# Kernel optimization log

Measured on AMD Instinct MI355X. Metric: run time of the kernel, lower is better.

The kernel has to match this reference:

```python
import jax, jax.numpy as jnp
import numpy as np

B, T, C, HS = 8, 4096, 512, 64

def setup_inputs() -> dict:
    key = jax.random.key(0)
    k1, k2, k3, k4 = jax.random.split(key, 4)
    x = jax.random.normal(k1, (B, T, C), dtype=jnp.float32)
    # causal mask (lower-triangular), int32: 1 = keep, 0 = mask out
    mask = jnp.tril(jnp.ones((T, T), dtype=jnp.int32))
    Wk = jax.random.normal(k2, (C, HS), dtype=jnp.float32) * (1.0 / np.sqrt(C))
    Wq = jax.random.normal(k3, (C, HS), dtype=jnp.float32) * (1.0 / np.sqrt(C))
    Wv = jax.random.normal(k4, (C, HS), dtype=jnp.float32) * (1.0 / np.sqrt(C))
    return {"x": x, "mask": mask, "Wk": Wk, "Wq": Wq, "Wv": Wv}

def reference(x, mask, Wk, Wq, Wv):
    # single self-attention head; scale uses C (n_embd), matching the source
    k = jnp.einsum('btc,ch->bth', x, Wk)   # [B,T,HS]
    q = jnp.einsum('btc,ch->bth', x, Wq)
    v = jnp.einsum('btc,ch->bth', x, Wv)
    scale = x.shape[-1] ** -0.5
    wei = jnp.einsum('bth,bsh->bts', q, k) * scale          # [B,T,T]
    wei = jnp.where(mask == 0, jnp.float32(-1e9), wei)
    wei = jax.nn.softmax(wei, axis=-1)
    # dropout is identity in eval mode
    out = jnp.einsum('bts,bsh->bth', wei, v)                # [B,T,HS]
    return out
```

## Files before the change

### kernel.cpp

```cpp
#include <hip/hip_runtime.h>
#include <hip/hip_bf16.h>
#include <stdint.h>

typedef unsigned short u16;
typedef __bf16 bf16x8_t __attribute__((ext_vector_type(8)));
typedef __bf16 bf16x4_t __attribute__((ext_vector_type(4)));
typedef float f32x4_t __attribute__((ext_vector_type(4)));
typedef float f32x8_t __attribute__((ext_vector_type(8)));
typedef float f32x16_t __attribute__((ext_vector_type(16)));
typedef int i32x2_t __attribute__((ext_vector_type(2)));

#define TSEQ 4096
#define CDIM 512
#define HSD  64
#define NBATCH 8

static __device__ __forceinline__ f32x4_t mfma16(bf16x8_t a, bf16x8_t b, f32x4_t c) {
  return __builtin_amdgcn_mfma_f32_16x16x32_bf16(a, b, c, 0, 0, 0);
}
static __device__ __forceinline__ f32x16_t mfma32(bf16x8_t a, bf16x8_t b, f32x16_t c) {
  return __builtin_amdgcn_mfma_f32_32x32x16_bf16(a, b, c, 0, 0, 0);
}

static __device__ __forceinline__ u16 f2bf(float f) {
  union { __bf16 h; u16 s; } v; v.h = (__bf16)f;
  return v.s;
}
static __device__ __forceinline__ float bf2f(u16 h) {
  union { unsigned u; float f; } v; v.u = ((unsigned)h) << 16;
  return v.f;
}
static __device__ __forceinline__ bf16x8_t pack8(const float* p) {
  f32x8_t v = *(const f32x8_t*)p;
  return __builtin_convertvector(v, bf16x8_t);
}
static __device__ __forceinline__ bf16x4_t cvt4(f32x4_t v) {
  return __builtin_convertvector(v, bf16x4_t);
}

static __device__ __forceinline__ void gload16(const void* g, void* l) {
  __builtin_amdgcn_global_load_lds(
      (const __attribute__((address_space(1))) unsigned int*)g,
      (__attribute__((address_space(3))) unsigned int*)l, 16, 0, 0);
}

#define QSCALE (0.044194173824159216f * 1.4426950408889634f)
#define MFIX 32.0f

__global__ __launch_bounds__(256) void repack_w(const float* __restrict__ Wk,
                                                const float* __restrict__ Wq,
                                                const float* __restrict__ Wv,
                                                u16* __restrict__ pw) {
  int i = blockIdx.x * 256 + threadIdx.x;
  int j    = i & 7;
  int l15  = (i >> 3) & 15;
  int quad = (i >> 7) & 3;
  int f    = i >> 9;
  int kc   = f / 12;
  int n12  = f - kc * 12;
  int m    = n12 >> 2;
  int n    = n12 & 3;
  const float* W = (m == 0) ? Wk : ((m == 1) ? Wq : Wv);
  pw[i] = f2bf(W[(kc * 32 + quad * 8 + j) * HSD + n * 16 + l15]);
}

__global__ __launch_bounds__(256, 2) void proj_kernel(const float* __restrict__ x,
                                                      const u16* __restrict__ pw,
                                                      u16* __restrict__ kb,
                                                      u16* __restrict__ qb,
                                                      u16* __restrict__ vb,
                                                      u16* __restrict__ vbT,
                                                      int split) {
  const int tid = threadIdx.x;
  const int lane = tid & 63;
  const int wave = tid >> 6;
  const int l15 = lane & 15, quad = lane >> 4;
  const int rblk = (int)blockIdx.x;
  const int rowLocal = wave * 16 + l15;

  __shared__ __align__(16) char SMEM[61440];
  float (*XS)[2048] = (float (*)[2048])SMEM;
  u16   (*PS)[6144] = (u16 (*)[6144])(SMEM + 24576);
  u16* VtS = (u16*)SMEM;

  const float* xg = x + (size_t)rblk * 64 * CDIM;

  const int xrow = tid >> 3;
  const int xch  = tid & 7;

  f32x4_t acc[12];
#pragma unroll
  for (int n = 0; n < 12; ++n) acc[n] = f32x4_t{0.f, 0.f, 0.f, 0.f};

  auto STAGE = [&](int slot, int kc) {
#pragma unroll
    for (int p = 0; p < 2; ++p) {
      const float* src = xg + (size_t)(p * 32 + xrow) * CDIM + kc * 32 + xch * 4;
      gload16(src, (char*)&XS[slot][0] + p * 4096 + tid * 16);
    }
#pragma unroll
    for (int r = 0; r < 3; ++r) {
      int f = r * 256 + tid;
      gload16(pw + (size_t)kc * 6144 + (size_t)f * 8, (char*)&PS[slot][0] + f * 16);
    }
  };

  STAGE(0, 0);
  STAGE(1, 1);

  int slot = 0;
  for (int kc = 0; kc < 16; ++kc) {
    if (kc < 15) asm volatile("s_waitcnt vmcnt(5)" ::: "memory");
    else         asm volatile("s_waitcnt vmcnt(0)" ::: "memory");
    __builtin_amdgcn_s_barrier();

    if (kc + 2 < 16) {
      int s2 = slot + 2; if (s2 >= 3) s2 -= 3;
      STAGE(s2, kc + 2);
    }

    f32x8_t xv = *(const f32x8_t*)&XS[slot][rowLocal * 32 + quad * 8];
    bf16x8_t a = __builtin_convertvector(xv, bf16x8_t);
#pragma unroll
    for (int n12 = 0; n12 < 12; ++n12) {
      bf16x8_t b = *(const bf16x8_t*)&PS[slot][((n12 * 4 + quad) * 16 + l15) * 8];
      acc[n12] = mfma16(a, b, acc[n12]);
    }

    ++slot; if (slot >= 3) slot = 0;
  }

  const int row_base = rblk * 64 + wave * 16 + quad * 4;
#pragma unroll
  for (int n = 0; n < 4; ++n) {
#pragma unroll
    for (int r = 0; r < 4; ++r) {
      kb[(size_t)(row_base + r) * HSD + n * 16 + l15] = f2bf(acc[n][r]);
      qb[(size_t)(row_base + r) * HSD + n * 16 + l15] = f2bf(acc[4 + n][r] * QSCALE);
    }
  }

  if (!split) {
#pragma unroll
    for (int n = 0; n < 4; ++n)
#pragma unroll
      for (int r = 0; r < 4; ++r)
        vb[(size_t)(row_base + r) * HSD + n * 16 + l15] = f2bf(acc[8 + n][r]);
  } else {
    __syncthreads();
#pragma unroll
    for (int n = 0; n < 4; ++n) {
      int h = n * 16 + l15;
      int tl = wave * 16 + quad * 4;
      *(bf16x4_t*)&VtS[h * 72 + tl] = cvt4(acc[8 + n]);
    }
    __syncthreads();
    const int bb = (rblk * 64) >> 12;
    const int t0 = (rblk * 64) & 4095;
#pragma unroll
    for (int it = 0; it < 2; ++it) {
      int g = it * 256 + tid;
      int h = g >> 3;
      int cc = g & 7;
      bf16x8_t vv = *(const bf16x8_t*)&VtS[h * 72 + cc * 8];
      *(bf16x8_t*)&vbT[(size_t)(bb * HSD + h) * TSEQ + t0 + cc * 8] = vv;
    }
  }
}

__global__ __launch_bounds__(256, 4) void attn_part(const u16* __restrict__ qb,
                                                    const u16* __restrict__ kb,
                                                    const u16* __restrict__ vbT,
                                                    u16* __restrict__ pO,
                                                    float* __restrict__ pl) {
  const int e = 143 - (int)blockIdx.x;
  int g = 0;
  while (g < 7 && 2 * (g + 1) * (g + 2) <= e) ++g;
  int local = e - 2 * g * (g + 1);
  int qtl = 0;
  while (local >= g + 1) { local -= g + 1; ++qtl; }
  const int qt2 = 4 * g + qtl;
  const int c   = local;

  const int b = blockIdx.y;
  const int tid = threadIdx.x;
  const int lane = tid & 63;
  const int wave = tid >> 6;
  const int l31 = lane & 31;
  const int h2  = lane >> 5;

  __shared__ __align__(16) u16 Ks[128 * 72];
  __shared__ __align__(16) u16 Vt[64 * 136];

  const size_t bo = (size_t)b * TSEQ * HSD;
  const u16* qp = qb + bo;
  const u16* kp = kb + bo;
  const u16* vtp = vbT + (size_t)b * HSD * TSEQ;

  const int qglob = qt2 * 128 + wave * 32 + l31;
  const int wdiag = (qt2 * 128 + wave * 32 + 31) >> 6;

  bf16x8_t qf[4];
#pragma unroll
  for (int kk = 0; kk < 4; ++kk)
    qf[kk] = *(const bf16x8_t*)(qp + (size_t)qglob * HSD + kk * 16 + h2 * 8);

  f32x16_t o0, o1;
#pragma unroll
  for (int i = 0; i < 16; ++i) { o0[i] = 0.f; o1[i] = 0.f; }
  float lsum = 0.f;

  const int st_lo = c * 8;
  const int nt = min(2 * qt2 + 2 - st_lo, 8);
  const int npair = (nt + 1) >> 1;

  const int kr = tid >> 3;
  const int kc8 = (tid & 7) * 8;
  const int vr = tid >> 4;
  const int vc8 = (tid & 15) * 8;

  bf16x8_t kst[4], vst[4];
  {
    const int s64 = st_lo * 64;
#pragma unroll
    for (int p = 0; p < 4; ++p) {
      kst[p] = *(const bf16x8_t*)(kp + (size_t)(s64 + kr + 32 * p) * HSD + kc8);
      vst[p] = *(const bf16x8_t*)(vtp + (size_t)(vr + 16 * p) * TSEQ + s64 + vc8);
    }
  }

  for (int ip = 0; ip < npair; ++ip) {
    __syncthreads();
#pragma unroll
    for (int p = 0; p < 4; ++p) {
      *(bf16x8_t*)&Ks[(kr + 32 * p) * 72 + kc8] = kst[p];
      *(bf16x8_t*)&Vt[(vr + 16 * p) * 136 + vc8] = vst[p];
    }
    if (ip + 1 < npair) {
      const int s64 = (st_lo + 2 * (ip + 1)) * 64;
#pragma unroll
      for (int p = 0; p < 4; ++p) {
        kst[p] = *(const bf16x8_t*)(kp + (size_t)(s64 + kr + 32 * p) * HSD + kc8);
        vst[p] = *(const bf16x8_t*)(vtp + (size_t)(vr + 16 * p) * TSEQ + s64 + vc8);
      }
    }
    __syncthreads();

    const int st0 = st_lo + 2 * ip;
    const int nsub = (2 * ip + 1 < nt) ? 2 : 1;
#pragma unroll 2
    for (int hs = 0; hs < nsub; ++hs) {
      const int stx = st0 + hs;
      if (stx > wdiag) continue;
      const int roff = hs * 64;

#pragma unroll
      for (int st2 = 0; st2 < 2; ++st2) {
        f32x16_t s;
#pragma unroll
        for (int i = 0; i < 16; ++i) s[i] = -MFIX;
#pragma unroll
        for (int kk = 0; kk < 4; ++kk) {
          bf16x8_t a = *(const bf16x8_t*)&Ks[(roff + st2 * 32 + l31) * 72 + kk * 16 + h2 * 8];
          s = mfma32(a, qf[kk], s);
        }

        if (stx == wdiag) {
#pragma unroll
          for (int i = 0; i < 16; ++i) {
            int sg = stx * 64 + st2 * 32 + 4 * h2 + (i & 3) + 8 * (i >> 2);
            if (sg > qglob) s[i] = -1e9f;
          }
        }

#pragma unroll
        for (int i = 0; i < 16; ++i) s[i] = exp2f(s[i]);
#pragma unroll
        for (int i = 0; i < 16; i += 4)
          lsum += ((s[i] + s[i + 1]) + (s[i + 2] + s[i + 3]));

        union { bf16x4_t v; int d[2]; } X[4];
#pragma unroll
        for (int m = 0; m < 4; ++m) {
          f32x4_t t;
          t[0] = s[4 * m]; t[1] = s[4 * m + 1]; t[2] = s[4 * m + 2]; t[3] = s[4 * m + 3];
          X[m].v = cvt4(t);
        }

#pragma unroll
        for (int kkl = 0; kkl < 2; ++kkl) {
          i32x2_t r0 = __builtin_amdgcn_permlane32_swap(X[2 * kkl].d[0], X[2 * kkl + 1].d[0], false, false);
          i32x2_t r1 = __builtin_amdgcn_permlane32_swap(X[2 * kkl].d[1], X[2 * kkl + 1].d[1], false, false);
          union { bf16x8_t v; int d[4]; } af;
          af.d[0] = r0[0]; af.d[1] = r1[0];
          af.d[2] = r0[1]; af.d[3] = r1[1];
          const int kkg = st2 * 2 + kkl;
          bf16x8_t vf0 = *(const bf16x8_t*)&Vt[l31 * 136 + roff + kkg * 16 + h2 * 8];
          bf16x8_t vf1 = *(const bf16x8_t*)&Vt[(32 + l31) * 136 + roff + kkg * 16 + h2 * 8];
          o0 = mfma32(af.v, vf0, o0);
          o1 = mfma32(af.v, vf1, o1);
        }
      }
    }
  }

  lsum += __shfl_xor(lsum, 32);

  const int pidx = (b * 64 + 2 * qt2 + (wave >> 1)) * 8 + c;
  u16* po = pO + (size_t)pidx * 4096;
  float* pm = pl + (size_t)pidx * 64;
#pragma unroll
  for (int i = 0; i < 16; ++i) {
    int rloc = (wave & 1) * 32 + 4 * h2 + (i & 3) + 8 * (i >> 2);
    po[rloc * 64 + l31]      = f2bf(o0[i]);
    po[rloc * 64 + 32 + l31] = f2bf(o1[i]);
  }
  if (lane < 32) pm[(wave & 1) * 32 + lane] = lsum;
}

__global__ __launch_bounds__(256) void attn_combine(const u16* __restrict__ pO,
                                                    const float* __restrict__ pl,
                                                    float* __restrict__ out) {
  const int tid = threadIdx.x;
  const int h2 = tid & 31;
  const int rr = tid >> 5;
  const int rowg = blockIdx.x * 8 + rr;
  const int b = rowg >> 12;
  const int t = rowg & 4095;
  const int qt = t >> 6;
  const int tr = t & 63;
  const int nc = (qt >> 3) + 1;
  const int pbase = (b * 64 + qt) * 8;

  const unsigned* pO32 = (const unsigned*)pO;
  float o0 = 0.f, o1 = 0.f, lsum = 0.f;
  for (int cc = 0; cc < nc; ++cc) {
    lsum += pl[(size_t)(pbase + cc) * 64 + tr];
    unsigned u = pO32[(size_t)(pbase + cc) * 2048 + tr * 32 + h2];
    o0 += bf2f((u16)(u & 0xffffu));
    o1 += bf2f((u16)(u >> 16));
  }
  float2 res;
  res.x = o0 / lsum;
  res.y = o1 / lsum;
  *(float2*)&out[(size_t)rowg * HSD + h2 * 2] = res;
}

__global__ __launch_bounds__(256) void attn_single(const u16* __restrict__ qb,
                                                   const u16* __restrict__ kb,
                                                   const u16* __restrict__ vb,
                                                   float* __restrict__ out) {
  const int qt = (int)gridDim.x - 1 - (int)blockIdx.x;
  const int b = blockIdx.y;
  const int lane = threadIdx.x & 63;
  const int wave = threadIdx.x >> 6;
  const int l15 = lane & 15, quad = lane >> 4;

  __shared__ __align__(16) u16 Ks[64 * 72];
  __shared__ __align__(16) u16 Vt[64 * 72];
  __shared__ __align__(16) u16 Ps[4][16 * 72];

  const size_t bo = (size_t)b * TSEQ * HSD;
  const u16* qp = qb + bo;
  const u16* kp = kb + bo;
  const u16* vp = vb + bo;

  const int qrow0 = qt * 64 + wave * 16;
  bf16x8_t qf0 = *(const bf16x8_t*)(qp + (size_t)(qrow0 + l15) * HSD + quad * 8);
  bf16x8_t qf1 = *(const bf16x8_t*)(qp + (size_t)(qrow0 + l15) * HSD + 32 + quad * 8);

  f32x4_t o[4];
#pragma unroll
  for (int n = 0; n < 4; ++n) o[n] = f32x4_t{0.f, 0.f, 0.f, 0.f};
  float lrow[4] = {0.f, 0.f, 0.f, 0.f};

  const int ldr = threadIdx.x >> 3;
  const int ldc = (threadIdx.x & 7) * 8;

  const f32x4_t sinit = f32x4_t{-MFIX, -MFIX, -MFIX, -MFIX};

  for (int st = 0; st <= qt; ++st) {
    const int s0 = st * 64;
#pragma unroll
    for (int pp = 0; pp < 2; ++pp) {
      int r = ldr + pp * 32;
      bf16x8_t kv = *(const bf16x8_t*)(kp + (size_t)(s0 + r) * HSD + ldc);
      *(bf16x8_t*)&Ks[r * 72 + ldc] = kv;
      bf16x8_t vv = *(const bf16x8_t*)(vp + (size_t)(s0 + r) * HSD + ldc);
      const u16* vu = (const u16*)&vv;
#pragma unroll
      for (int j = 0; j < 8; ++j) Vt[(ldc + j) * 72 + r] = vu[j];
    }
    __syncthreads();

    f32x4_t s[4];
#pragma unroll
    for (int n = 0; n < 4; ++n) {
      bf16x8_t k0 = *(const bf16x8_t*)&Ks[(n * 16 + l15) * 72 + quad * 8];
      bf16x8_t k1 = *(const bf16x8_t*)&Ks[(n * 16 + l15) * 72 + 32 + quad * 8];
      f32x4_t a = sinit;
      a = mfma16(qf0, k0, a);
      a = mfma16(qf1, k1, a);
      s[n] = a;
    }

    if (st == qt) {
#pragma unroll
      for (int n = 0; n < 4; ++n) {
        int sg = s0 + n * 16 + l15;
#pragma unroll
        for (int r = 0; r < 4; ++r) {
          int tg = qrow0 + quad * 4 + r;
          if (sg > tg) s[n][r] = -1e9f;
        }
      }
    }

#pragma unroll
    for (int n = 0; n < 4; ++n)
#pragma unroll
      for (int r = 0; r < 4; ++r) {
        float p = exp2f(s[n][r]);
        s[n][r] = p;
        lrow[r] += p;
      }

    u16* myP = Ps[wave];
#pragma unroll
    for (int n = 0; n < 4; ++n)
#pragma unroll
      for (int r = 0; r < 4; ++r)
        myP[(quad * 4 + r) * 72 + n * 16 + l15] = f2bf(s[n][r]);

    __syncthreads();

#pragma unroll
    for (int kc = 0; kc < 2; ++kc) {
      bf16x8_t pf = *(const bf16x8_t*)&myP[l15 * 72 + kc * 32 + quad * 8];
#pragma unroll
      for (int n = 0; n < 4; ++n) {
        bf16x8_t vf = *(const bf16x8_t*)&Vt[(n * 16 + l15) * 72 + kc * 32 + quad * 8];
        o[n] = mfma16(pf, vf, o[n]);
      }
    }
    __syncthreads();
  }

#pragma unroll
  for (int r = 0; r < 4; ++r) {
    float l = lrow[r];
    l += __shfl_xor(l, 1);
    l += __shfl_xor(l, 2);
    l += __shfl_xor(l, 4);
    l += __shfl_xor(l, 8);
    lrow[r] = l;
  }

#pragma unroll
  for (int n = 0; n < 4; ++n)
#pragma unroll
    for (int r = 0; r < 4; ++r)
      out[bo + (size_t)(qrow0 + quad * 4 + r) * HSD + n * 16 + l15] = o[n][r] / lrow[r];
}

extern "C" void kernel_launch(void* const* d_in, const int* in_sizes, int n_in,
                              void* d_out, int out_size, void* d_ws, size_t ws_size,
                              hipStream_t stream) {
  const float* x  = (const float*)d_in[0];
  const float* Wk = (const float*)d_in[2];
  const float* Wq = (const float*)d_in[3];
  const float* Wv = (const float*)d_in[4];
  float* out = (float*)d_out;

  char* base = (char*)d_ws;
  const size_t KV = (size_t)NBATCH * TSEQ * HSD;
  u16* pw  = (u16*)base;
  u16* kb  = (u16*)(base + (1 << 18));
  u16* qb  = kb + KV;
  u16* vbT = qb + KV;
  u16* pO  = vbT + KV;
  u16* vb  = pO;
  float* pl = (float*)(pO + (size_t)4096 * 4096);
  const size_t need = (size_t)(1 << 18) + 3 * KV * 2
                    + (size_t)4096 * 4096 * 2
                    + (size_t)4096 * 64 * 4;
  const int split = (ws_size >= need) ? 1 : 0;

  hipLaunchKernelGGL(repack_w, dim3(384), dim3(256), 0, stream, Wk, Wq, Wv, pw);
  hipLaunchKernelGGL(proj_kernel, dim3(512), dim3(256), 0, stream, x, pw, kb, qb, vb, vbT, split);
  if (split) {
    hipLaunchKernelGGL(attn_part, dim3(144, NBATCH), dim3(256), 0, stream, qb, kb, vbT, pO, pl);
    hipLaunchKernelGGL(attn_combine, dim3(4096), dim3(256), 0, stream, pO, pl, out);
  } else {
    hipLaunchKernelGGL(attn_single, dim3(64, NBATCH), dim3(256), 0, stream, qb, kb, vb, out);
  }
}
```

Before: 215.1 us.

## Stream K/V tiles into swizzled LDS via direct global-to-LDS double buffering

The attention partial kernel stops staging K and V^T tiles through registers and padded shared arrays. It now uses global_load_lds DMA into two double-buffered 64-row tiles with an XOR-swizzled layout, prefetching two tiles ahead. Raw s_waitcnt vmcnt and s_barrier calls order the copies against compute. This is meant to cut register pressure and the VGPR-to-LDS store traffic and to overlap loads with MFMA work, at the cost of one barrier pair per 64-key tile instead of per pair of tiles, plus fragile hand-counted waitcnt logic.

New measurement: 191.5 us. 11.0% less time.

```diff
diff --git a/kernel.cpp b/kernel.cpp
--- a/kernel.cpp
+++ b/kernel.cpp
@@ -29,10 +29,6 @@
 static __device__ __forceinline__ float bf2f(u16 h) {
   union { unsigned u; float f; } v; v.u = ((unsigned)h) << 16;
   return v.f;
-}
-static __device__ __forceinline__ bf16x8_t pack8(const float* p) {
-  f32x8_t v = *(const f32x8_t*)p;
-  return __builtin_convertvector(v, bf16x8_t);
 }
 static __device__ __forceinline__ bf16x4_t cvt4(f32x4_t v) {
   return __builtin_convertvector(v, bf16x4_t);
@@ -189,8 +185,7 @@
   const int l31 = lane & 31;
   const int h2  = lane >> 5;
 
-  __shared__ __align__(16) u16 Ks[128 * 72];
-  __shared__ __align__(16) u16 Vt[64 * 136];
+  __shared__ __align__(16) char LDS[32768];
 
   const size_t bo = (size_t)b * TSEQ * HSD;
   const u16* qp = qb + bo;
@@ -212,48 +207,44 @@
 
   const int st_lo = c * 8;
   const int nt = min(2 * qt2 + 2 - st_lo, 8);
-  const int npair = (nt + 1) >> 1;
-
-  const int kr = tid >> 3;
-  const int kc8 = (tid & 7) * 8;
-  const int vr = tid >> 4;
-  const int vc8 = (tid & 15) * 8;
-
-  bf16x8_t kst[4], vst[4];
-  {
-    const int s64 = st_lo * 64;
-#pragma unroll
-    for (int p = 0; p < 4; ++p) {
-      kst[p] = *(const bf16x8_t*)(kp + (size_t)(s64 + kr + 32 * p) * HSD + kc8);
-      vst[p] = *(const bf16x8_t*)(vtp + (size_t)(vr + 16 * p) * TSEQ + s64 + vc8);
-    }
-  }
-
-  for (int ip = 0; ip < npair; ++ip) {
-    __syncthreads();
-#pragma unroll
-    for (int p = 0; p < 4; ++p) {
-      *(bf16x8_t*)&Ks[(kr + 32 * p) * 72 + kc8] = kst[p];
-      *(bf16x8_t*)&Vt[(vr + 16 * p) * 136 + vc8] = vst[p];
-    }
-    if (ip + 1 < npair) {
-      const int s64 = (st_lo + 2 * (ip + 1)) * 64;
-#pragma unroll
-      for (int p = 0; p < 4; ++p) {
-        kst[p] = *(const bf16x8_t*)(kp + (size_t)(s64 + kr + 32 * p) * HSD + kc8);
-        vst[p] = *(const bf16x8_t*)(vtp + (size_t)(vr + 16 * p) * TSEQ + s64 + vc8);
-      }
-    }
-    __syncthreads();
-
-    const int st0 = st_lo + 2 * ip;
-    const int nsub = (2 * ip + 1 < nt) ? 2 : 1;
-#pragma unroll 2
-    for (int hs = 0; hs < nsub; ++hs) {
-      const int stx = st0 + hs;
-      if (stx > wdiag) continue;
-      const int roff = hs * 64;
-
+
+  const int c0 = l31 & 7;
+  int A[4];
+#pragma unroll
+  for (int j = 0; j < 4; ++j) A[j] = l31 * 128 + (((j * 2 + h2) ^ c0) << 4);
+
+  const u16* ksrc[2];
+  const u16* vsrc[2];
+#pragma unroll
+  for (int i = 0; i < 2; ++i) {
+    int q = wave * 128 + i * 64 + lane;
+    int row = q >> 3, cl = (q & 7) ^ (row & 7);
+    ksrc[i] = kp + (size_t)(st_lo * 64 + row) * HSD + cl * 8;
+    vsrc[i] = vtp + (size_t)row * TSEQ + st_lo * 64 + cl * 8;
+  }
+
+  auto DMA = [&](int t) {
+    const int buf = t & 1;
+    char* kd = LDS + buf * 8192 + wave * 2048;
+    char* vd = LDS + 16384 + buf * 8192 + wave * 2048;
+    gload16(ksrc[0] + (size_t)t * 64 * HSD, kd);
+    gload16(ksrc[1] + (size_t)t * 64 * HSD, kd + 1024);
+    gload16(vsrc[0] + (size_t)t * 64, vd);
+    gload16(vsrc[1] + (size_t)t * 64, vd + 1024);
+  };
+
+  DMA(0);
+  DMA(1);
+
+  auto TILE = [&](int t, int buf) {
+    if (t + 1 < nt) asm volatile("s_waitcnt vmcnt(4)" ::: "memory");
+    else            asm volatile("s_waitcnt vmcnt(0)" ::: "memory");
+    __builtin_amdgcn_s_barrier();
+
+    const int stx = st_lo + t;
+    if (stx <= wdiag) {
+      const char* kbase = LDS + buf * 8192;
+      const char* vbase = LDS + 16384 + buf * 8192;
 #pragma unroll
       for (int st2 = 0; st2 < 2; ++st2) {
         f32x16_t s;
@@ -261,7 +252,7 @@
         for (int i = 0; i < 16; ++i) s[i] = -MFIX;
 #pragma unroll
         for (int kk = 0; kk < 4; ++kk) {
-          bf16x8_t a = *(const bf16x8_t*)&Ks[(roff + st2 * 32 + l31) * 72 + kk * 16 + h2 * 8];
+          bf16x8_t a = *(const bf16x8_t*)(kbase + st2 * 4096 + A[kk]);
           s = mfma32(a, qf[kk], s);
         }
 
@@ -282,9 +273,9 @@
         union { bf16x4_t v; int d[2]; } X[4];
 #pragma unroll
         for (int m = 0; m < 4; ++m) {
-          f32x4_t t;
-          t[0] = s[4 * m]; t[1] = s[4 * m + 1]; t[2] = s[4 * m + 2]; t[3] = s[4 * m + 3];
-          X[m].v = cvt4(t);
+          f32x4_t tt;
+          tt[0] = s[4 * m]; tt[1] = s[4 * m + 1]; tt[2] = s[4 * m + 2]; tt[3] = s[4 * m + 3];
+          X[m].v = cvt4(tt);
         }
 
 #pragma unroll
@@ -295,13 +286,21 @@
           af.d[0] = r0[0]; af.d[1] = r1[0];
           af.d[2] = r0[1]; af.d[3] = r1[1];
           const int kkg = st2 * 2 + kkl;
-          bf16x8_t vf0 = *(const bf16x8_t*)&Vt[l31 * 136 + roff + kkg * 16 + h2 * 8];
-          bf16x8_t vf1 = *(const bf16x8_t*)&Vt[(32 + l31) * 136 + roff + kkg * 16 + h2 * 8];
+          bf16x8_t vf0 = *(const bf16x8_t*)(vbase + A[kkg]);
+          bf16x8_t vf1 = *(const bf16x8_t*)(vbase + 4096 + A[kkg]);
           o0 = mfma32(af.v, vf0, o0);
           o1 = mfma32(af.v, vf1, o1);
         }
       }
     }
+
+    __builtin_amdgcn_s_barrier();
+    if (t + 2 < nt) DMA(t + 2);
+  };
+
+  for (int ip = 0; ip < (nt >> 1); ++ip) {
+    TILE(2 * ip, 0);
+    TILE(2 * ip + 1, 1);
   }
 
   lsum += __shfl_xor(lsum, 32);
```
